# Kernel tuning notes

Hardware: AMD Instinct MI355X
Metric: run time of the kernel (lower is better)

Reference implementation:

```python
import jax, jax.numpy as jnp
import numpy as np

N_HEADS = 8
N_POINTS = 4
LN_EPS = 1e-5


def _ln(x, g, b):
    m = jnp.mean(x, -1, keepdims=True)
    v = jnp.mean((x - m) ** 2, -1, keepdims=True)
    return (x - m) * jax.lax.rsqrt(v + LN_EPS) * g + b


def _mha(q, k, v, wq, bq, wk, bk, wv, bv, wo, bo):
    B, Lq, C = q.shape
    Dh = C // N_HEADS
    Q = (q @ wq.T + bq).reshape(B, Lq, N_HEADS, Dh)
    K = (k @ wk.T + bk).reshape(B, -1, N_HEADS, Dh)
    V = (v @ wv.T + bv).reshape(B, -1, N_HEADS, Dh)
    s = jnp.einsum('bqhd,bkhd->bhqk', Q, K) * (1.0 / float(np.sqrt(Dh)))
    a = jax.nn.softmax(s, -1)
    o = jnp.einsum('bhqk,bkhd->bqhd', a, V).reshape(B, Lq, C)
    return o @ wo.T + bo


def _ref_points(h, w, L):
    ry = jnp.linspace(0.5, h - 0.5, h) / h
    rx = jnp.linspace(0.5, w - 0.5, w) / w
    gy, gx = jnp.meshgrid(ry, rx, indexing='ij')
    ref = jnp.stack([gx.reshape(-1), gy.reshape(-1)], -1)[None]  # (1, h*w, 2)
    return jnp.broadcast_to(ref[:, :, None, :], (1, h * w, L, 2))


def _deform_core(value, shapes, starts, loc, aw):
    # value: (B, Len_in, H, Dh); loc: (B, Lq, H, L, P, 2); aw: (B, Lq, H, L, P)
    B, _, H, Dh = value.shape
    Lq, P = loc.shape[1], loc.shape[4]
    out = jnp.zeros((B, H, Lq, Dh), value.dtype)
    for l in range(shapes.shape[0]):
        Hl, Wl = int(shapes[l, 0]), int(shapes[l, 1])
        s = int(starts[l])
        v = value[:, s:s + Hl * Wl].transpose(0, 2, 1, 3)  # (B, H, Hl*Wl, Dh)
        # grid_sample(align_corners=False, padding_mode='zeros') pixel coords
        xl = loc[:, :, :, l, :, 0] * Wl - 0.5  # (B, Lq, H, P)
        yl = loc[:, :, :, l, :, 1] * Hl - 0.5
        x0 = jnp.floor(xl); y0 = jnp.floor(yl)
        fx = xl - x0; fy = yl - y0
        x0 = x0.astype(jnp.int32); y0 = y0.astype(jnp.int32)
        acc = jnp.zeros((B, H, Lq, P, Dh), value.dtype)
        for dy, dx in ((0, 0), (0, 1), (1, 0), (1, 1)):
            xi = x0 + dx; yi = y0 + dy
            wgt = (fx if dx else 1.0 - fx) * (fy if dy else 1.0 - fy)
            valid = ((xi >= 0) & (xi < Wl) & (yi >= 0) & (yi < Hl)).astype(value.dtype)
            idx = (jnp.clip(yi, 0, Hl - 1) * Wl + jnp.clip(xi, 0, Wl - 1))
            idx = idx.transpose(0, 2, 1, 3).reshape(B, H, Lq * P)
            g = jnp.take_along_axis(v, idx[..., None], axis=2).reshape(B, H, Lq, P, Dh)
            acc = acc + g * (wgt * valid).transpose(0, 2, 1, 3)[..., None]
        out = out + jnp.einsum('bhqpd,bqhp->bhqd', acc, aw[:, :, :, l])
    return out.transpose(0, 2, 1, 3).reshape(B, Lq, H * Dh)


def reference(tgt, query_pos, src, wq, bq, wk, bk, wv, bv, wo, bo, ln2_g, ln2_b,
              w_off, b_off, w_attn, b_attn, w_val, b_val, w_cout, b_cout,
              ln1_g, ln1_b, w1, b1, w2, b2, ln3_g, ln3_b,
              src_spatial_shapes, level_start_index, h, w):
    shapes = np.asarray(src_spatial_shapes)
    starts = np.asarray(level_start_index)
    h = int(h); w = int(w)
    L = shapes.shape[0]
    B, Lq, C = tgt.shape
    Dh = C // N_HEADS
    # --- self attention (post-LN residual) ---
    q = tgt + query_pos
    t2 = _mha(q, q, tgt, wq, bq, wk, bk, wv, bv, wo, bo)
    t = _ln(tgt + t2, ln2_g, ln2_b)
    # --- MSDeformAttn cross attention ---
    qc = t + query_pos
    value = (src @ w_val.T + b_val).reshape(B, -1, N_HEADS, Dh)
    off = (qc @ w_off.T + b_off).reshape(B, Lq, N_HEADS, L, N_POINTS, 2)
    aw = (qc @ w_attn.T + b_attn).reshape(B, Lq, N_HEADS, L * N_POINTS)
    aw = jax.nn.softmax(aw, -1).reshape(B, Lq, N_HEADS, L, N_POINTS)
    norm = jnp.stack([shapes[:, 1].astype(np.float32), shapes[:, 0].astype(np.float32)], -1)  # (L,2): (W,H)
    rp = _ref_points(h, w, L)  # (1, Lq, L, 2)
    loc = rp[:, :, None, :, None, :] + off / norm[None, None, None, :, None, :]
    samp = _deform_core(value, shapes, starts, loc, aw)
    t2 = samp @ w_cout.T + b_cout
    t = _ln(t + t2, ln1_g, ln1_b)
    # --- FFN ---
    t2 = jax.nn.relu(t @ w1.T + b1) @ w2.T + b2
    t = _ln(t + t2, ln3_g, ln3_b)
    return t


def setup_inputs() -> dict:
    key = jax.random.key(0)
    B, C, L, P, dff = 2, 256, 4, 4, 1024
    h = w = 48
    shapes = np.array([[48, 48], [24, 24], [12, 12], [6, 6]], np.int32)
    starts = np.array([0, 2304, 2880, 3024], np.int32)
    Len_in = 3060
    Lq = h * w
    ks = iter(jax.random.split(key, 40))
    def rn(shape, s=0.02):
        return jax.random.normal(next(ks), shape, jnp.float32) * s
    return dict(
        tgt=rn((B, Lq, C), 1.0), query_pos=rn((B, Lq, C), 1.0), src=rn((B, Len_in, C), 1.0),
        wq=rn((C, C)), bq=rn((C,)), wk=rn((C, C)), bk=rn((C,)), wv=rn((C, C)), bv=rn((C,)),
        wo=rn((C, C)), bo=rn((C,)),
        ln2_g=jnp.ones((C,)), ln2_b=jnp.zeros((C,)),
        w_off=rn((N_HEADS * L * P * 2, C)), b_off=rn((N_HEADS * L * P * 2,)),
        w_attn=rn((N_HEADS * L * P, C)), b_attn=rn((N_HEADS * L * P,)),
        w_val=rn((C, C)), b_val=rn((C,)), w_cout=rn((C, C)), b_cout=rn((C,)),
        ln1_g=jnp.ones((C,)), ln1_b=jnp.zeros((C,)),
        w1=rn((dff, C)), b1=rn((dff,)), w2=rn((C, dff)), b2=rn((C,)),
        ln3_g=jnp.ones((C,)), ln3_b=jnp.zeros((C,)),
        src_spatial_shapes=shapes, level_start_index=starts, h=h, w=w)
```

## Files before the change

kernel.cpp:

```cpp
#include <hip/hip_runtime.h>
#include <hip/hip_bf16.h>
#include <math.h>

typedef __hip_bfloat16 bf16;
typedef __attribute__((ext_vector_type(8))) short short8;
typedef __attribute__((ext_vector_type(4))) short short4v;
typedef __attribute__((ext_vector_type(4))) float f32x4;

static constexpr int B   = 2;
static constexpr int LQ  = 2304;
static constexpr int C   = 256;
static constexpr int NH  = 8;
static constexpr int DH  = 32;
static constexpr int NL  = 4;
static constexpr int NP  = 4;
static constexpr int LEN = 3060;
static constexpr int DFF = 1024;
static constexpr int MQ  = B * LQ;
static constexpr int MV  = B * LEN;
static constexpr int SZ1 = MQ * C;

#define MFMA16(a, b, c) __builtin_amdgcn_mfma_f32_16x16x32_bf16(a, b, c, 0, 0, 0)

__device__ __forceinline__ float ldf(const void* p, size_t i, int bf) {
  return bf ? __bfloat162float(((const bf16*)p)[i]) : ((const float*)p)[i];
}
__device__ __forceinline__ short fl2s(float v) {
  bf16 h = __float2bfloat16(v);
  return *(short*)&h;
}
__device__ __forceinline__ short fl2s_fast(float v) {
  union { float f; unsigned u; } x; x.f = v;
  return (short)((x.u + 0x8000u) >> 16);
}
__device__ __forceinline__ float s2fl(short s) {
  return __bfloat162float(*(bf16*)&s);
}
__device__ __forceinline__ int wire_is_bf16(const unsigned* gprobe) {
  return gprobe[0] == 0x3F803F80u;
}

static constexpr int CVN = 20;
__device__ const int g_cvt_cnt[CVN] = {
  65536, 65536, 256, 256, 65536, 256, 65536, 256,
  65536, 32768, 256, 128, 65536, 256, 65536, 256,
  262144, 1024, 262144, 256};
__device__ const int g_cvt_off[CVN] = {
  0, 65536, 131072, 131328, 131584, 197120, 197376, 262912,
  263168, 328704, 361472, 361728, 361856, 427392, 427648, 493184,
  493440, 755584, 756608, 1018752};
static constexpr int CV_WQ = 0, CV_BQ = 131072, CV_WV = 131584, CV_BV = 197120;
static constexpr int CV_WO = 197376, CV_BO = 262912;
static constexpr int CV_WOFF = 263168, CV_BOFF = 361472;
static constexpr int CV_WVAL = 361856, CV_BVAL = 427392;
static constexpr int CV_WCOUT = 427648, CV_BCOUT = 493184;
static constexpr int CV_W1 = 493440, CV_B1 = 755584;
static constexpr int CV_W2 = 756608, CV_B2 = 1018752;
static constexpr int CV_TOTAL = 1019008;

struct CvtArgs { const void* p[22]; };

__global__ __launch_bounds__(256) void prep_all(CvtArgs a, const void* __restrict__ qpos,
                                                short* __restrict__ cvt,
                                                short* __restrict__ tgt16,
                                                short* __restrict__ q16,
                                                short* __restrict__ src16,
                                                const unsigned* __restrict__ gprobe) {
  const int fl = wire_is_bf16(gprobe);
  const int seg = blockIdx.y;
  if (fl && seg < 20 && !((seg <= 3) || (seg >= 8 && seg <= 11))) return;
  const int cnt = (seg < 20) ? g_cvt_cnt[seg] : (seg == 20 ? SZ1 : MV * C);
  const int stride = gridDim.x * 256;
  for (int i = blockIdx.x * 256 + threadIdx.x; i < cnt; i += stride) {
    if (seg < 20) {
      cvt[g_cvt_off[seg] + i] = fl ? ((const short*)a.p[seg])[i]
                                   : fl2s(((const float*)a.p[seg])[i]);
    } else if (seg == 20) {
      float t = ldf(a.p[20], i, fl);
      tgt16[i] = fl2s(t);
      q16[i] = fl2s(t + ldf(qpos, i, fl));
    } else {
      src16[i] = fl ? ((const short*)a.p[21])[i] : fl2s(((const float*)a.p[21])[i]);
    }
  }
}

struct GemmJob {
  const short* X; const short* W; const short* bias; void* Y;
  const void* Wwire; const void* bwire;
  int M, N, K, relu, out_mode, nblk_x;
  float qscale; int qscaleN;
};
struct GemmBatch { GemmJob j[3]; int start[4]; int njobs; };

__global__ __launch_bounds__(256) void gemm_mfma(GemmBatch nb,
                                                 const unsigned* __restrict__ gprobe) {
  const int fl = wire_is_bf16(gprobe);
  int id = blockIdx.x;
  int jj = 0;
  while (jj + 1 < nb.njobs && id >= nb.start[jj + 1]) ++jj;
  const GemmJob jb = nb.j[jj];
  const short* Wsel = (jb.Wwire && fl) ? (const short*)jb.Wwire : jb.W;
  const short* bsel = (jb.bwire && fl) ? (const short*)jb.bwire : jb.bias;
  const int local = id - nb.start[jj];
  const int bx = local % jb.nblk_x;
  const int by = local / jb.nblk_x;
  const int M = jb.M, N = jb.N, K = jb.K;

  __shared__ short Xs[64][72];
  __shared__ short Ws[64][72];
  const int tid = threadIdx.x;
  const int wave = tid >> 6, lane = tid & 63;
  const int quad = lane >> 4, l16 = lane & 15;
  const int m0 = bx * 64, n0 = by * 64;
  f32x4 acc[4] = {{0.f,0.f,0.f,0.f},{0.f,0.f,0.f,0.f},{0.f,0.f,0.f,0.f},{0.f,0.f,0.f,0.f}};

  const int srow = tid >> 2;
  const int scol = (tid & 3) * 16;
  int xr = m0 + srow; if (xr >= M) xr = M - 1;
  const short* xp = jb.X + (size_t)xr * K;
  const short* wp = Wsel + (size_t)(n0 + srow) * K;

  for (int k0 = 0; k0 < K; k0 += 64) {
    *(short8*)&Xs[srow][scol]     = *(const short8*)(xp + k0 + scol);
    *(short8*)&Xs[srow][scol + 8] = *(const short8*)(xp + k0 + scol + 8);
    *(short8*)&Ws[srow][scol]     = *(const short8*)(wp + k0 + scol);
    *(short8*)&Ws[srow][scol + 8] = *(const short8*)(wp + k0 + scol + 8);
    __syncthreads();
#pragma unroll
    for (int kc = 0; kc < 2; ++kc) {
      short8 a = *(const short8*)&Xs[wave * 16 + l16][kc * 32 + quad * 8];
#pragma unroll
      for (int nt = 0; nt < 4; ++nt) {
        short8 b = *(const short8*)&Ws[nt * 16 + l16][kc * 32 + quad * 8];
        acc[nt] = MFMA16(a, b, acc[nt]);
      }
    }
    __syncthreads();
  }

  if (jb.out_mode == 2) {
    const int mbase = m0 + wave * 16 + quad * 4;
    const int b = mbase / LQ;
    const int qb_ = mbase - b * LQ;
#pragma unroll
    for (int nt = 0; nt < 4; ++nt) {
      const int n = n0 + nt * 16 + l16;
      const float bv = s2fl(bsel[n]);
      short4v v4;
#pragma unroll
      for (int r = 0; r < 4; ++r) v4[r] = fl2s(acc[nt][r] + bv);
      *(short4v*)((short*)jb.Y + (size_t)(b * 256 + n) * LQ + qb_) = v4;
    }
    return;
  }
#pragma unroll
  for (int nt = 0; nt < 4; ++nt) {
    const int n = n0 + nt * 16 + l16;
    const float bv = s2fl(bsel[n]);
    const float sc = (n < jb.qscaleN) ? jb.qscale : 1.f;
#pragma unroll
    for (int r = 0; r < 4; ++r) {
      const int m = m0 + wave * 16 + quad * 4 + r;
      if (m < M) {
        float v = (acc[nt][r] + bv) * sc;
        if (jb.relu) v = fmaxf(v, 0.f);
        if (jb.out_mode == 1) ((short*)jb.Y)[(size_t)m * N + n] = fl2s(v);
        else ((float*)jb.Y)[(size_t)m * N + n] = v;
      }
    }
  }
}

__global__ __launch_bounds__(256) void flash_attn(const short* __restrict__ QK,
                                                  const short* __restrict__ Vt,
                                                  short* __restrict__ Op) {
  constexpr int LDQK = 512;
  constexpr int NC = LQ / 64;
  constexpr int NQT = 3;
  const int qb = blockIdx.x;
  const int bh = blockIdx.y;
  const int b = bh >> 3, h = bh & 7;
  const int tid = threadIdx.x;
  const int wave = tid >> 6, lane = tid & 63;
  const int quad = lane >> 4, l16 = lane & 15;

  __shared__ short Ps[4][16][68];
  __shared__ float lsh[256];

  const int q0 = qb * 48;
  const size_t rowb = (size_t)(b * LQ);
  const short* kcol = QK + 256 + h * DH + quad * 8;
  const short* vt0 = Vt + (size_t)(b * 256 + h * 32 + l16) * LQ + quad * 8;
  const short* vt1 = Vt + (size_t)(b * 256 + h * 32 + 16 + l16) * LQ + quad * 8;

  short8 qfrag[NQT];
#pragma unroll
  for (int qt = 0; qt < NQT; ++qt)
    qfrag[qt] = *(const short8*)(QK + (rowb + q0 + qt * 16 + l16) * LDQK + h * DH + quad * 8);

  f32x4 o0[NQT], o1[NQT];
  float lrow[NQT];
#pragma unroll
  for (int qt = 0; qt < NQT; ++qt) {
    o0[qt] = f32x4{0.f, 0.f, 0.f, 0.f};
    o1[qt] = f32x4{0.f, 0.f, 0.f, 0.f};
    lrow[qt] = 0.f;
  }

  short8 kf[4], vf[4];
  {
    const int k0 = wave * 64;
#pragma unroll
    for (int kt = 0; kt < 4; ++kt)
      kf[kt] = *(const short8*)(kcol + (rowb + k0 + kt * 16 + l16) * LDQK);
    vf[0] = *(const short8*)(vt0 + k0);
    vf[1] = *(const short8*)(vt0 + k0 + 32);
    vf[2] = *(const short8*)(vt1 + k0);
    vf[3] = *(const short8*)(vt1 + k0 + 32);
  }

  for (int c = wave; c < NC; c += 4) {
    short8 kn[4], vn[4];
    if (c + 4 < NC) {
      const int k0n = (c + 4) * 64;
#pragma unroll
      for (int kt = 0; kt < 4; ++kt)
        kn[kt] = *(const short8*)(kcol + (rowb + k0n + kt * 16 + l16) * LDQK);
      vn[0] = *(const short8*)(vt0 + k0n);
      vn[1] = *(const short8*)(vt0 + k0n + 32);
      vn[2] = *(const short8*)(vt1 + k0n);
      vn[3] = *(const short8*)(vt1 + k0n + 32);
    }

#pragma unroll
    for (int qt = 0; qt < NQT; ++qt) {
      f32x4 s[4];
#pragma unroll
      for (int kt = 0; kt < 4; ++kt) {
        f32x4 z = {0.f, 0.f, 0.f, 0.f};
        s[kt] = MFMA16(kf[kt], qfrag[qt], z);
      }

      float ps = 0.f;
#pragma unroll
      for (int kt = 0; kt < 4; ++kt)
#pragma unroll
        for (int r = 0; r < 4; ++r) {
          float p = __expf(s[kt][r]);
          s[kt][r] = p;
          ps += p;
        }
      lrow[qt] += ps;

#pragma unroll
      for (int kt = 0; kt < 4; ++kt) {
        short4v pk;
#pragma unroll
        for (int r = 0; r < 4; ++r) pk[r] = fl2s_fast(s[kt][r]);
        *(short4v*)&Ps[wave][l16][kt * 16 + quad * 4] = pk;
      }

#pragma unroll
      for (int half = 0; half < 2; ++half) {
        short4v a0 = *(const short4v*)&Ps[wave][l16][half * 32 + quad * 8];
        short4v a1 = *(const short4v*)&Ps[wave][l16][half * 32 + quad * 8 + 4];
        short8 afrag;
#pragma unroll
        for (int j = 0; j < 4; ++j) { afrag[j] = a0[j]; afrag[4 + j] = a1[j]; }
        o0[qt] = MFMA16(afrag, vf[half], o0[qt]);
        o1[qt] = MFMA16(afrag, vf[2 + half], o1[qt]);
      }
    }

#pragma unroll
    for (int kt = 0; kt < 4; ++kt) { kf[kt] = kn[kt]; vf[kt] = vn[kt]; }
  }

  float* obuf = (float*)&Ps[0][0][0];
  for (int qt = 0; qt < NQT; ++qt) {
    __syncthreads();
    lsh[(wave * 4 + quad) * 16 + l16] = lrow[qt];
#pragma unroll
    for (int r = 0; r < 4; ++r) {
      const int q = quad * 4 + r;
      obuf[(wave * 16 + q) * 32 + l16] = o0[qt][r];
      obuf[(wave * 16 + q) * 32 + 16 + l16] = o1[qt][r];
    }
    __syncthreads();
#pragma unroll
    for (int e = tid; e < 512; e += 256) {
      const int q = e >> 5, d = e & 31;
      float lg = 0.f;
#pragma unroll
      for (int i = 0; i < 16; ++i) lg += lsh[i * 16 + q];
      float ov = 0.f;
#pragma unroll
      for (int w = 0; w < 4; ++w) ov += obuf[(w * 16 + q) * 32 + d];
      Op[(rowb + q0 + qt * 16 + q) * C + h * DH + d] = fl2s_fast(ov / lg);
    }
  }
}

__global__ __launch_bounds__(256) void ln_kern(const void* __restrict__ A, int a_mode,
                                               const float* __restrict__ R,
                                               const void* __restrict__ g,
                                               const void* __restrict__ be,
                                               float* __restrict__ Yf32,
                                               short* __restrict__ Y16,
                                               void* __restrict__ Yfinal,
                                               const void* __restrict__ pos,
                                               short* __restrict__ Yqc,
                                               int rows, const unsigned* __restrict__ gprobe) {
  const int fl = wire_is_bf16(gprobe);
  const int row = blockIdx.x * 4 + (threadIdx.x >> 6);
  const int lane = threadIdx.x & 63;
  if (row >= rows) return;
  float x[4], s = 0.f, s2 = 0.f;
#pragma unroll
  for (int u = 0; u < 4; ++u) {
    int c = lane + 64 * u;
    size_t idx = (size_t)row * C + c;
    float a = (a_mode == 1) ? ldf(A, idx, fl) : ((const float*)A)[idx];
    x[u] = a + R[idx];
    s += x[u];
    s2 += x[u] * x[u];
  }
#pragma unroll
  for (int off = 32; off > 0; off >>= 1) {
    s += __shfl_xor(s, off);
    s2 += __shfl_xor(s2, off);
  }
  const float mean = s * (1.f / C);
  const float var = fmaxf(s2 * (1.f / C) - mean * mean, 0.f);
  const float inv = rsqrtf(var + 1e-5f);
#pragma unroll
  for (int u = 0; u < 4; ++u) {
    int c = lane + 64 * u;
    size_t idx = (size_t)row * C + c;
    float y = (x[u] - mean) * inv * ldf(g, c, fl) + ldf(be, c, fl);
    if (Yfinal) {
      if (fl) ((short*)Yfinal)[idx] = fl2s(y);
      else ((float*)Yfinal)[idx] = y;
    } else {
      if (Yf32) Yf32[idx] = y;
      if (Y16) Y16[idx] = fl2s(y);
      if (Yqc) Yqc[idx] = fl2s(y + ldf(pos, idx, fl));
    }
  }
}

__global__ __launch_bounds__(256) void deform_kern(const short* __restrict__ value,
                                                   const float* __restrict__ oa,
                                                   const int* __restrict__ shapes,
                                                   const int* __restrict__ starts,
                                                   const int* __restrict__ hp,
                                                   const int* __restrict__ wp,
                                                   short* __restrict__ samp) {
  const int bq = blockIdx.x * 4 + (threadIdx.x >> 6);
  const int b = bq / LQ, q = bq % LQ;
  const int lane = threadIdx.x & 63;
  const int h_ = lane >> 3;
  const int d0 = (lane & 7) * 4;

  const int w0 = *wp, h0 = *hp;
  const int qx = q % w0, qy = q / w0;
  const float refx = (qx + 0.5f) / (float)w0;
  const float refy = (qy + 0.5f) / (float)h0;

  const float* offp = oa + (size_t)bq * 384 + h_ * 32;
  const float* awraw = oa + (size_t)bq * 384 + 256 + h_ * 16;

  float e[16];
  float mm = -1e30f;
#pragma unroll
  for (int j = 0; j < 16; ++j) mm = fmaxf(mm, awraw[j]);
  float ssum = 0.f;
#pragma unroll
  for (int j = 0; j < 16; ++j) {
    e[j] = __expf(awraw[j] - mm);
    ssum += e[j];
  }
  const float sinv = 1.f / ssum;

  float acc0 = 0.f, acc1 = 0.f, acc2 = 0.f, acc3 = 0.f;
  for (int l = 0; l < NL; ++l) {
    const int Hl = shapes[l * 2 + 0];
    const int Wl = shapes[l * 2 + 1];
    const int st = starts[l];
    const short* vbase = value + ((size_t)(b * LEN + st)) * C + h_ * DH + d0;
#pragma unroll
    for (int p = 0; p < NP; ++p) {
      const float ox = offp[l * 8 + p * 2 + 0];
      const float oy = offp[l * 8 + p * 2 + 1];
      const float a = e[l * 4 + p] * sinv;
      const float xl = refx * Wl + ox - 0.5f;
      const float yl = refy * Hl + oy - 0.5f;
      const float x0f = floorf(xl), y0f = floorf(yl);
      const float fx = xl - x0f, fy = yl - y0f;
      const int x0 = (int)x0f, y0 = (int)y0f;
#pragma unroll
      for (int corner = 0; corner < 4; ++corner) {
        const int dx = corner & 1, dy = corner >> 1;
        const int xi = x0 + dx, yi = y0 + dy;
        const float wx = dx ? fx : 1.f - fx;
        const float wy = dy ? fy : 1.f - fy;
        const bool valid = (xi >= 0) & (xi < Wl) & (yi >= 0) & (yi < Hl);
        if (valid) {
          const float w = a * wx * wy;
          short4v v4 = *(const short4v*)(vbase + (size_t)(yi * Wl + xi) * C);
          acc0 += w * s2fl(v4[0]);
          acc1 += w * s2fl(v4[1]);
          acc2 += w * s2fl(v4[2]);
          acc3 += w * s2fl(v4[3]);
        }
      }
    }
  }
  short4v out;
  out[0] = fl2s(acc0); out[1] = fl2s(acc1); out[2] = fl2s(acc2); out[3] = fl2s(acc3);
  *(short4v*)(samp + (size_t)bq * C + h_ * DH + d0) = out;
}

extern "C" void kernel_launch(void* const* d_in, const int* in_sizes, int n_in,
                              void* d_out, int out_size, void* d_ws, size_t ws_size,
                              hipStream_t stream) {
  const void* tgt       = d_in[0];
  const void* query_pos = d_in[1];
  const void* src       = d_in[2];
  const void* wq = d_in[3];  const void* bq = d_in[4];
  const void* wk = d_in[5];  const void* bk = d_in[6];
  const void* wv = d_in[7];  const void* bv = d_in[8];
  const void* wo = d_in[9];  const void* bo = d_in[10];
  const void* ln2_g = d_in[11]; const void* ln2_b = d_in[12];
  const void* w_off = d_in[13]; const void* b_off = d_in[14];
  const void* w_attn = d_in[15]; const void* b_attn = d_in[16];
  const void* w_val = d_in[17]; const void* b_val = d_in[18];
  const void* w_cout = d_in[19]; const void* b_cout = d_in[20];
  const void* ln1_g = d_in[21]; const void* ln1_b = d_in[22];
  const void* w1 = d_in[23]; const void* b1 = d_in[24];
  const void* w2 = d_in[25]; const void* b2 = d_in[26];
  const void* ln3_g = d_in[27]; const void* ln3_b = d_in[28];
  const int* shapes = (const int*)d_in[29];
  const int* starts = (const int*)d_in[30];
  const int* hp = (const int*)d_in[31];
  const int* wp = (const int*)d_in[32];
  const unsigned* gprobe = (const unsigned*)ln2_g;

  short* cvt    = (short*)((char*)d_ws + 256);
  short* tgt16  = cvt + CV_TOTAL;
  short* q16    = tgt16 + SZ1;
  short* src16  = q16 + SZ1;
  short* qk_out = src16 + (size_t)MV * C;
  short* vt16   = qk_out + (size_t)MQ * 512;
  short* ao16   = vt16 + SZ1;
  short* valb   = ao16 + SZ1;
  short* ffn1   = valb + (size_t)MV * C;
  short* t1_16  = ffn1 + (size_t)MQ * DFF;
  float* t2a    = (float*)(t1_16 + SZ1);
  float* t_32   = t2a + SZ1;
  float* t1_32  = t_32 + SZ1;
  float* oa     = t1_32 + SZ1;

  const float scale = 1.f / sqrtf((float)DH);
  const dim3 blk(256);

  CvtArgs ca;
  ca.p[0] = wq;  ca.p[1] = wk;  ca.p[2] = bq;  ca.p[3] = bk;
  ca.p[4] = wv;  ca.p[5] = bv;  ca.p[6] = wo;  ca.p[7] = bo;
  ca.p[8] = w_off; ca.p[9] = w_attn; ca.p[10] = b_off; ca.p[11] = b_attn;
  ca.p[12] = w_val; ca.p[13] = b_val; ca.p[14] = w_cout; ca.p[15] = b_cout;
  ca.p[16] = w1; ca.p[17] = b1; ca.p[18] = w2; ca.p[19] = b2;
  ca.p[20] = tgt; ca.p[21] = src;
  prep_all<<<dim3(192, 22), blk, 0, stream>>>(ca, query_pos, cvt, tgt16, q16, src16, gprobe);

  {
    GemmBatch nb;
    nb.njobs = 3;
    nb.j[0] = {q16, cvt + CV_WQ, cvt + CV_BQ, qk_out, nullptr, nullptr,
               MQ, 512, 256, 0, 1, MQ / 64, scale, 256};
    nb.j[1] = {tgt16, cvt + CV_WV, cvt + CV_BV, vt16, wv, bv,
               MQ, 256, 256, 0, 2, MQ / 64, 1.f, 0};
    nb.j[2] = {src16, cvt + CV_WVAL, cvt + CV_BVAL, valb, w_val, b_val,
               MV, 256, 256, 0, 1, (MV + 63) / 64, 1.f, 0};
    nb.start[0] = 0;
    nb.start[1] = (MQ / 64) * 8;
    nb.start[2] = nb.start[1] + (MQ / 64) * 4;
    nb.start[3] = nb.start[2] + ((MV + 63) / 64) * 4;
    gemm_mfma<<<nb.start[3], blk, 0, stream>>>(nb, gprobe);
  }
  flash_attn<<<dim3(LQ / 48, B * NH), blk, 0, stream>>>(qk_out, vt16, ao16);
  {
    GemmBatch nb;
    nb.njobs = 1;
    nb.j[0] = {ao16, cvt + CV_WO, cvt + CV_BO, t2a, wo, bo,
               MQ, 256, 256, 0, 0, MQ / 64, 1.f, 0};
    nb.start[0] = 0; nb.start[1] = (MQ / 64) * 4;
    gemm_mfma<<<nb.start[1], blk, 0, stream>>>(nb, gprobe);
  }
  ln_kern<<<MQ / 4, blk, 0, stream>>>(tgt, 1, t2a, ln2_g, ln2_b,
                                      t_32, nullptr, nullptr, query_pos, q16, MQ, gprobe);

  {
    GemmBatch nb;
    nb.njobs = 1;
    nb.j[0] = {q16, cvt + CV_WOFF, cvt + CV_BOFF, oa, nullptr, nullptr,
               MQ, 384, 256, 0, 0, MQ / 64, 1.f, 0};
    nb.start[0] = 0; nb.start[1] = (MQ / 64) * 6;
    gemm_mfma<<<nb.start[1], blk, 0, stream>>>(nb, gprobe);
  }
  deform_kern<<<MQ / 4, blk, 0, stream>>>(valb, oa, shapes, starts, hp, wp, ao16);
  {
    GemmBatch nb;
    nb.njobs = 1;
    nb.j[0] = {ao16, cvt + CV_WCOUT, cvt + CV_BCOUT, t2a, w_cout, b_cout,
               MQ, 256, 256, 0, 0, MQ / 64, 1.f, 0};
    nb.start[0] = 0; nb.start[1] = (MQ / 64) * 4;
    gemm_mfma<<<nb.start[1], blk, 0, stream>>>(nb, gprobe);
  }
  ln_kern<<<MQ / 4, blk, 0, stream>>>(t_32, 2, t2a, ln1_g, ln1_b,
                                      t1_32, t1_16, nullptr, nullptr, nullptr, MQ, gprobe);

  {
    GemmBatch nb;
    nb.njobs = 1;
    nb.j[0] = {t1_16, cvt + CV_W1, cvt + CV_B1, ffn1, w1, b1,
               MQ, 1024, 256, 1, 1, MQ / 64, 1.f, 0};
    nb.start[0] = 0; nb.start[1] = (MQ / 64) * 16;
    gemm_mfma<<<nb.start[1], blk, 0, stream>>>(nb, gprobe);
  }
  {
    GemmBatch nb;
    nb.njobs = 1;
    nb.j[0] = {ffn1, cvt + CV_W2, cvt + CV_B2, t2a, w2, b2,
               MQ, 256, 1024, 0, 0, MQ / 64, 1.f, 0};
    nb.start[0] = 0; nb.start[1] = (MQ / 64) * 4;
    gemm_mfma<<<nb.start[1], blk, 0, stream>>>(nb, gprobe);
  }
  ln_kern<<<MQ / 4, blk, 0, stream>>>(t1_32, 2, t2a, ln3_g, ln3_b,
                                      nullptr, nullptr, d_out, nullptr, nullptr, MQ, gprobe);
}
```

Before: 285.1 us.

## Use 128-row GEMM tiles and read bf16 wire inputs directly instead of copying

The GEMM tile grows from 64x64 to 128x64, with each wave computing two 16-row M subtiles. Each B tile is now reused across twice as many rows. GEMM jobs gain column offsets and leading dimensions, so fused outputs like QK and offset/attention are split into per-weight jobs writing into a shared buffer. When the inputs already arrive as bf16, prep no longer copies weights, tgt or src; the GEMM reads the wire tensors directly. The trade-off is half as many blocks per launch, which may lower occupancy or parallelism on the small GEMMs.

Measured after the change: 284.2 us. No clear change (-0.3%).

```diff
diff --git a/kernel.cpp b/kernel.cpp
--- a/kernel.cpp
+++ b/kernel.cpp
@@ -49,9 +49,11 @@
   0, 65536, 131072, 131328, 131584, 197120, 197376, 262912,
   263168, 328704, 361472, 361728, 361856, 427392, 427648, 493184,
   493440, 755584, 756608, 1018752};
-static constexpr int CV_WQ = 0, CV_BQ = 131072, CV_WV = 131584, CV_BV = 197120;
+static constexpr int CV_WQ = 0, CV_WK = 65536, CV_BQ = 131072, CV_BK = 131328;
+static constexpr int CV_WV = 131584, CV_BV = 197120;
 static constexpr int CV_WO = 197376, CV_BO = 262912;
-static constexpr int CV_WOFF = 263168, CV_BOFF = 361472;
+static constexpr int CV_WOFF = 263168, CV_WATTN = 328704;
+static constexpr int CV_BOFF = 361472, CV_BATTN = 361728;
 static constexpr int CV_WVAL = 361856, CV_BVAL = 427392;
 static constexpr int CV_WCOUT = 427648, CV_BCOUT = 493184;
 static constexpr int CV_W1 = 493440, CV_B1 = 755584;
@@ -68,30 +70,32 @@
                                                 const unsigned* __restrict__ gprobe) {
   const int fl = wire_is_bf16(gprobe);
   const int seg = blockIdx.y;
-  if (fl && seg < 20 && !((seg <= 3) || (seg >= 8 && seg <= 11))) return;
+  if (fl && seg != 20) return;
   const int cnt = (seg < 20) ? g_cvt_cnt[seg] : (seg == 20 ? SZ1 : MV * C);
   const int stride = gridDim.x * 256;
   for (int i = blockIdx.x * 256 + threadIdx.x; i < cnt; i += stride) {
     if (seg < 20) {
-      cvt[g_cvt_off[seg] + i] = fl ? ((const short*)a.p[seg])[i]
-                                   : fl2s(((const float*)a.p[seg])[i]);
+      cvt[g_cvt_off[seg] + i] = fl2s(((const float*)a.p[seg])[i]);
     } else if (seg == 20) {
       float t = ldf(a.p[20], i, fl);
-      tgt16[i] = fl2s(t);
+      if (!fl) tgt16[i] = fl2s(t);
       q16[i] = fl2s(t + ldf(qpos, i, fl));
     } else {
-      src16[i] = fl ? ((const short*)a.p[21])[i] : fl2s(((const float*)a.p[21])[i]);
+      src16[i] = fl2s(((const float*)a.p[21])[i]);
     }
   }
 }
 
 struct GemmJob {
-  const short* X; const short* W; const short* bias; void* Y;
+  int Xmode;
+  const short* Xbf; const void* Xwire;
+  const short* Wcvt; const short* bcvt;
   const void* Wwire; const void* bwire;
-  int M, N, K, relu, out_mode, nblk_x;
-  float qscale; int qscaleN;
+  void* Y;
+  int M, N, K, ldY, col0, relu, out_mode, nblk_x;
+  float qscale;
 };
-struct GemmBatch { GemmJob j[3]; int start[4]; int njobs; };
+struct GemmBatch { GemmJob j[4]; int start[5]; int njobs; };
 
 __global__ __launch_bounds__(256) void gemm_mfma(GemmBatch nb,
                                                  const unsigned* __restrict__ gprobe) {
@@ -100,76 +104,93 @@
   int jj = 0;
   while (jj + 1 < nb.njobs && id >= nb.start[jj + 1]) ++jj;
   const GemmJob jb = nb.j[jj];
-  const short* Wsel = (jb.Wwire && fl) ? (const short*)jb.Wwire : jb.W;
-  const short* bsel = (jb.bwire && fl) ? (const short*)jb.bwire : jb.bias;
+  const short* Xsel = (jb.Xmode && fl) ? (const short*)jb.Xwire : jb.Xbf;
+  const short* Wsel = fl ? (const short*)jb.Wwire : jb.Wcvt;
+  const short* bsel = fl ? (const short*)jb.bwire : jb.bcvt;
   const int local = id - nb.start[jj];
   const int bx = local % jb.nblk_x;
   const int by = local / jb.nblk_x;
   const int M = jb.M, N = jb.N, K = jb.K;
 
-  __shared__ short Xs[64][72];
+  __shared__ short Xs[128][72];
   __shared__ short Ws[64][72];
   const int tid = threadIdx.x;
   const int wave = tid >> 6, lane = tid & 63;
   const int quad = lane >> 4, l16 = lane & 15;
-  const int m0 = bx * 64, n0 = by * 64;
-  f32x4 acc[4] = {{0.f,0.f,0.f,0.f},{0.f,0.f,0.f,0.f},{0.f,0.f,0.f,0.f},{0.f,0.f,0.f,0.f}};
-
-  const int srow = tid >> 2;
-  const int scol = (tid & 3) * 16;
-  int xr = m0 + srow; if (xr >= M) xr = M - 1;
-  const short* xp = jb.X + (size_t)xr * K;
-  const short* wp = Wsel + (size_t)(n0 + srow) * K;
+  const int m0 = bx * 128, n0 = by * 64;
+  f32x4 acc[2][4];
+#pragma unroll
+  for (int mt = 0; mt < 2; ++mt)
+#pragma unroll
+    for (int nt = 0; nt < 4; ++nt) acc[mt][nt] = f32x4{0.f, 0.f, 0.f, 0.f};
+
+  const int xrow = tid >> 1;
+  const int xcol = (tid & 1) * 32;
+  const int wrow = tid >> 2;
+  const int wcol = (tid & 3) * 16;
+  int xr = m0 + xrow; if (xr >= M) xr = M - 1;
+  const short* xp = Xsel + (size_t)xr * K;
+  const short* wp = Wsel + (size_t)(n0 + wrow) * K;
 
   for (int k0 = 0; k0 < K; k0 += 64) {
-    *(short8*)&Xs[srow][scol]     = *(const short8*)(xp + k0 + scol);
-    *(short8*)&Xs[srow][scol + 8] = *(const short8*)(xp + k0 + scol + 8);
-    *(short8*)&Ws[srow][scol]     = *(const short8*)(wp + k0 + scol);
-    *(short8*)&Ws[srow][scol + 8] = *(const short8*)(wp + k0 + scol + 8);
+#pragma unroll
+    for (int u = 0; u < 4; ++u)
+      *(short8*)&Xs[xrow][xcol + u * 8] = *(const short8*)(xp + k0 + xcol + u * 8);
+    *(short8*)&Ws[wrow][wcol]     = *(const short8*)(wp + k0 + wcol);
+    *(short8*)&Ws[wrow][wcol + 8] = *(const short8*)(wp + k0 + wcol + 8);
     __syncthreads();
 #pragma unroll
     for (int kc = 0; kc < 2; ++kc) {
-      short8 a = *(const short8*)&Xs[wave * 16 + l16][kc * 32 + quad * 8];
+#pragma unroll
+      for (int mt = 0; mt < 2; ++mt) {
+        short8 a = *(const short8*)&Xs[wave * 32 + mt * 16 + l16][kc * 32 + quad * 8];
+#pragma unroll
+        for (int nt = 0; nt < 4; ++nt) {
+          short8 b = *(const short8*)&Ws[nt * 16 + l16][kc * 32 + quad * 8];
+          acc[mt][nt] = MFMA16(a, b, acc[mt][nt]);
+        }
+      }
+    }
+    __syncthreads();
+  }
+
+  if (jb.out_mode == 2) {
+#pragma unroll
+    for (int mt = 0; mt < 2; ++mt) {
+      const int mbase = m0 + wave * 32 + mt * 16 + quad * 4;
+      const int b = mbase / LQ;
+      const int qb_ = mbase - b * LQ;
 #pragma unroll
       for (int nt = 0; nt < 4; ++nt) {
-        short8 b = *(const short8*)&Ws[nt * 16 + l16][kc * 32 + quad * 8];
-        acc[nt] = MFMA16(a, b, acc[nt]);
-      }
-    }
-    __syncthreads();
-  }
-
-  if (jb.out_mode == 2) {
-    const int mbase = m0 + wave * 16 + quad * 4;
-    const int b = mbase / LQ;
-    const int qb_ = mbase - b * LQ;
+        const int n = n0 + nt * 16 + l16;
+        const float bv = s2fl(bsel[n]);
+        short4v v4;
+#pragma unroll
+        for (int r = 0; r < 4; ++r) v4[r] = fl2s(acc[mt][nt][r] + bv);
+        *(short4v*)((short*)jb.Y + (size_t)(b * 256 + n) * LQ + qb_) = v4;
+      }
+    }
+    return;
+  }
+#pragma unroll
+  for (int mt = 0; mt < 2; ++mt)
 #pragma unroll
     for (int nt = 0; nt < 4; ++nt) {
       const int n = n0 + nt * 16 + l16;
       const float bv = s2fl(bsel[n]);
-      short4v v4;
-#pragma unroll
-      for (int r = 0; r < 4; ++r) v4[r] = fl2s(acc[nt][r] + bv);
-      *(short4v*)((short*)jb.Y + (size_t)(b * 256 + n) * LQ + qb_) = v4;
-    }
-    return;
-  }
-#pragma unroll
-  for (int nt = 0; nt < 4; ++nt) {
-    const int n = n0 + nt * 16 + l16;
-    const float bv = s2fl(bsel[n]);
-    const float sc = (n < jb.qscaleN) ? jb.qscale : 1.f;
-#pragma unroll
-    for (int r = 0; r < 4; ++r) {
-      const int m = m0 + wave * 16 + quad * 4 + r;
-      if (m < M) {
-        float v = (acc[nt][r] + bv) * sc;
-        if (jb.relu) v = fmaxf(v, 0.f);
-        if (jb.out_mode == 1) ((short*)jb.Y)[(size_t)m * N + n] = fl2s(v);
-        else ((float*)jb.Y)[(size_t)m * N + n] = v;
-      }
-    }
-  }
+#pragma unroll
+      for (int r = 0; r < 4; ++r) {
+        const int m = m0 + wave * 32 + mt * 16 + quad * 4 + r;
+        if (m < M) {
+          float v = (acc[mt][nt][r] + bv) * jb.qscale;
+          if (jb.relu) v = fmaxf(v, 0.f);
+          if (jb.out_mode == 1)
+            ((short*)jb.Y)[(size_t)m * jb.ldY + jb.col0 + n] = fl2s(v);
+          else
+            ((float*)jb.Y)[(size_t)m * jb.ldY + jb.col0 + n] = v;
+        }
+      }
+    }
 }
 
 __global__ __launch_bounds__(256) void flash_attn(const short* __restrict__ QK,
@@ -464,6 +485,8 @@
 
   const float scale = 1.f / sqrtf((float)DH);
   const dim3 blk(256);
+  const int NXQ = MQ / 128;
+  const int NXV = (MV + 127) / 128;
 
   CvtArgs ca;
   ca.p[0] = wq;  ca.p[1] = wk;  ca.p[2] = bq;  ca.p[3] = bk;
@@ -476,26 +499,29 @@
 
   {
     GemmBatch nb;
-    nb.njobs = 3;
-    nb.j[0] = {q16, cvt + CV_WQ, cvt + CV_BQ, qk_out, nullptr, nullptr,
-               MQ, 512, 256, 0, 1, MQ / 64, scale, 256};
-    nb.j[1] = {tgt16, cvt + CV_WV, cvt + CV_BV, vt16, wv, bv,
-               MQ, 256, 256, 0, 2, MQ / 64, 1.f, 0};
-    nb.j[2] = {src16, cvt + CV_WVAL, cvt + CV_BVAL, valb, w_val, b_val,
-               MV, 256, 256, 0, 1, (MV + 63) / 64, 1.f, 0};
+    nb.njobs = 4;
+    nb.j[0] = {0, q16, nullptr, cvt + CV_WQ, cvt + CV_BQ, wq, bq, qk_out,
+               MQ, 256, 256, 512, 0, 0, 1, NXQ, scale};
+    nb.j[1] = {0, q16, nullptr, cvt + CV_WK, cvt + CV_BK, wk, bk, qk_out,
+               MQ, 256, 256, 512, 256, 0, 1, NXQ, 1.f};
+    nb.j[2] = {2, tgt16, tgt, cvt + CV_WV, cvt + CV_BV, wv, bv, vt16,
+               MQ, 256, 256, 0, 0, 0, 2, NXQ, 1.f};
+    nb.j[3] = {3, src16, src, cvt + CV_WVAL, cvt + CV_BVAL, w_val, b_val, valb,
+               MV, 256, 256, 256, 0, 0, 1, NXV, 1.f};
     nb.start[0] = 0;
-    nb.start[1] = (MQ / 64) * 8;
-    nb.start[2] = nb.start[1] + (MQ / 64) * 4;
-    nb.start[3] = nb.start[2] + ((MV + 63) / 64) * 4;
-    gemm_mfma<<<nb.start[3], blk, 0, stream>>>(nb, gprobe);
+    nb.start[1] = NXQ * 4;
+    nb.start[2] = nb.start[1] + NXQ * 4;
+    nb.start[3] = nb.start[2] + NXQ * 4;
+    nb.start[4] = nb.start[3] + NXV * 4;
+    gemm_mfma<<<nb.start[4], blk, 0, stream>>>(nb, gprobe);
   }
   flash_attn<<<dim3(LQ / 48, B * NH), blk, 0, stream>>>(qk_out, vt16, ao16);
   {
     GemmBatch nb;
     nb.njobs = 1;
-    nb.j[0] = {ao16, cvt + CV_WO, cvt + CV_BO, t2a, wo, bo,
-               MQ, 256, 256, 0, 0, MQ / 64, 1.f, 0};
-    nb.start[0] = 0; nb.start[1] = (MQ / 64) * 4;
+    nb.j[0] = {0, ao16, nullptr, cvt + CV_WO, cvt + CV_BO, wo, bo, t2a,
+               MQ, 256, 256, 256, 0, 0, 0, NXQ, 1.f};
+    nb.start[0] = 0; nb.start[1] = NXQ * 4;
     gemm_mfma<<<nb.start[1], blk, 0, stream>>>(nb, gprobe);
   }
   ln_kern<<<MQ / 4, blk, 0, stream>>>(tgt, 1, t2a, ln2_g, ln2_b,
@@ -503,19 +529,23 @@
 
   {
     GemmBatch nb;
-    nb.njobs = 1;
-    nb.j[0] = {q16, cvt + CV_WOFF, cvt + CV_BOFF, oa, nullptr, nullptr,
-               MQ, 384, 256, 0, 0, MQ / 64, 1.f, 0};
-    nb.start[0] = 0; nb.start[1] = (MQ / 64) * 6;
-    gemm_mfma<<<nb.start[1], blk, 0, stream>>>(nb, gprobe);
+    nb.njobs = 2;
+    nb.j[0] = {0, q16, nullptr, cvt + CV_WOFF, cvt + CV_BOFF, w_off, b_off, oa,
+               MQ, 256, 256, 384, 0, 0, 0, NXQ, 1.f};
+    nb.j[1] = {0, q16, nullptr, cvt + CV_WATTN, cvt + CV_BATTN, w_attn, b_attn, oa,
+               MQ, 128, 256, 384, 256, 0, 0, NXQ, 1.f};
+    nb.start[0] = 0;
+    nb.start[1] = NXQ * 4;
+    nb.start[2] = nb.start[1] + NXQ * 2;
+    gemm_mfma<<<nb.start[2], blk, 0, stream>>>(nb, gprobe);
   }
   deform_kern<<<MQ / 4, blk, 0, stream>>>(valb, oa, shapes, starts, hp, wp, ao16);
   {
     GemmBatch nb;
     nb.njobs = 1;
-    nb.j[0] = {ao16, cvt + CV_WCOUT, cvt + CV_BCOUT, t2a, w_cout, b_cout,
-               MQ, 256, 256, 0, 0, MQ / 64, 1.f, 0};
-    nb.start[0] = 0; nb.start[1] = (MQ / 64) * 4;
+    nb.j[0] = {0, ao16, nullptr, cvt + CV_WCOUT, cvt + CV_BCOUT, w_cout, b_cout, t2a,
+               MQ, 256, 256, 256, 0, 0, 0, NXQ, 1.f};
+    nb.start[0] = 0; nb.start[1] = NXQ * 4;
     gemm_mfma<<<nb.start[1], blk, 0, stream>>>(nb, gprobe);
   }
   ln_kern<<<MQ / 4, blk, 0, stream>>>(t_32, 2, t2a, ln1_g, ln1_b,
@@ -524,17 +554,17 @@
   {
     GemmBatch nb;
     nb.njobs = 1;
-    nb.j[0] = {t1_16, cvt + CV_W1, cvt + CV_B1, ffn1, w1, b1,
-               MQ, 1024, 256, 1, 1, MQ / 64, 1.f, 0};
-    nb.start[0] = 0; nb.start[1] = (MQ / 64) * 16;
+    nb.j[0] = {0, t1_16, nullptr, cvt + CV_W1, cvt + CV_B1, w1, b1, ffn1,
+               MQ, 1024, 256, 1024, 0, 1, 1, NXQ, 1.f};
+    nb.start[0] = 0; nb.start[1] = NXQ * 16;
     gemm_mfma<<<nb.start[1], blk, 0, stream>>>(nb, gprobe);
   }
   {
     GemmBatch nb;
     nb.njobs = 1;
-    nb.j[0] = {ffn1, cvt + CV_W2, cvt + CV_B2, t2a, w2, b2,
-               MQ, 256, 1024, 0, 0, MQ / 64, 1.f, 0};
-    nb.start[0] = 0; nb.start[1] = (MQ / 64) * 4;
+    nb.j[0] = {0, ffn1, nullptr, cvt + CV_W2, cvt + CV_B2, w2, b2, t2a,
+               MQ, 256, 1024, 256, 0, 0, 0, NXQ, 1.f};
+    nb.start[0] = 0; nb.start[1] = NXQ * 4;
     gemm_mfma<<<nb.start[1], blk, 0, stream>>>(nb, gprobe);
   }
   ln_kern<<<MQ / 4, blk, 0, stream>>>(t1_32, 2, t2a, ln3_g, ln3_b,
```
